# Kernel tuning notes

Hardware: AMD Instinct MI355X
Metric: run time of the kernel (lower is better)

## Reference

```python
import jax, jax.numpy as jnp
import numpy as np

SEQ_LEN, BATCH, INPUT, HID, LAYERS, TARGET_LEN = 120, 2048, 6, 64, 4, 120


def _cell(x_t, h, c, Wih, Whh, b):
    # torch LSTM gate order: input, forget, cell(g), output
    gates = x_t @ Wih.T + h @ Whh.T + b  # [B, 4H]
    i, f, g, o = jnp.split(gates, 4, axis=-1)
    c_new = jax.nn.sigmoid(f) * c + jax.nn.sigmoid(i) * jnp.tanh(g)
    h_new = jax.nn.sigmoid(o) * jnp.tanh(c_new)
    return h_new, c_new


def _stack_step(h, c, x_t, Wih0, Wih, Whh, b):
    # one time step through all stacked layers; h, c: [L, B, H]
    hs, cs = [], []
    inp = x_t
    L = Whh.shape[0]
    for l in range(L):
        W = Wih0 if l == 0 else Wih[l - 1]
        hn, cn = _cell(inp, h[l], c[l], W, Whh[l], b[l])
        hs.append(hn)
        cs.append(cn)
        inp = hn
    return jnp.stack(hs), jnp.stack(cs), inp


def setup_inputs() -> dict:
    key = jax.random.key(0)
    ks = jax.random.split(key, 11)
    s = 1.0 / np.sqrt(HID)  # torch LSTM uniform init scale
    u = lambda k, shp: jax.random.uniform(k, shp, jnp.float32, -s, s)
    return {
        "x": jax.random.normal(ks[0], (SEQ_LEN, BATCH, INPUT), jnp.float32),
        "enc_Wih0": u(ks[1], (4 * HID, INPUT)),
        "enc_Wih": u(ks[2], (LAYERS - 1, 4 * HID, HID)),
        "enc_Whh": u(ks[3], (LAYERS, 4 * HID, HID)),
        "enc_b": u(ks[4], (LAYERS, 4 * HID)),
        "dec_Wih0": u(ks[5], (4 * HID, INPUT)),
        "dec_Wih": u(ks[6], (LAYERS - 1, 4 * HID, HID)),
        "dec_Whh": u(ks[7], (LAYERS, 4 * HID, HID)),
        "dec_b": u(ks[8], (LAYERS, 4 * HID)),
        "lin_W": u(ks[9], (INPUT, HID)),
        "lin_b": u(ks[10], (INPUT,)),
        "target_len": TARGET_LEN,
    }


def reference(x, enc_Wih0, enc_Wih, enc_Whh, enc_b,
              dec_Wih0, dec_Wih, dec_Whh, dec_b, lin_W, lin_b, target_len):
    L, B, H = enc_Whh.shape[0], x.shape[1], enc_Whh.shape[-1]
    h0 = jnp.zeros((L, B, H), x.dtype)

    # ---- encoder: stacked LSTM over the input sequence (zero init state) ----
    def enc_step(carry, x_t):
        h, c = carry
        h, c, _ = _stack_step(h, c, x_t, enc_Wih0, enc_Wih, enc_Whh, enc_b)
        return (h, c), None

    (h, c), _ = jax.lax.scan(enc_step, (h0, h0), x)

    # ---- decoder: recursive one-step decode for target_len steps ----
    def dec_step(carry, _):
        h, c, inp = carry
        h, c, top = _stack_step(h, c, inp, dec_Wih0, dec_Wih, dec_Whh, dec_b)
        out = top @ lin_W.T + lin_b  # [B, INPUT]
        return (h, c, out), out

    last_in = x[-1]  # decoder seeded with last observed frame
    _, outputs = jax.lax.scan(dec_step, (h, c, last_in), None, length=target_len)
    return outputs  # [target_len, B, INPUT]
```

## Files before the change

kernel.cpp:

```cpp
#include <hip/hip_runtime.h>


#define S_LEN 120
#define BATCH 2048
#define NIN   6
#define H     64
#define NL    4
#define TLEN  120

#define HPAD 72
#define XPAD 40

#define FRAGS_HALF 60
#define PACK_H8    (2 * FRAGS_HALF * 4 * 64)
#define PROJ_H8    (2 * 64)
#define NPACK      ((PACK_H8 + PROJ_H8) * 8)

typedef _Float16 h8    __attribute__((ext_vector_type(8)));
typedef float    f32x4 __attribute__((ext_vector_type(4)));

__global__ void prep_weights(const float* __restrict__ eWih0,
                             const float* __restrict__ eWih,
                             const float* __restrict__ eWhh,
                             const float* __restrict__ dWih0,
                             const float* __restrict__ dWih,
                             const float* __restrict__ dWhh,
                             const float* __restrict__ linW,
                             _Float16* __restrict__ wq) {
  int idx = blockIdx.x * blockDim.x + threadIdx.x;
  if (idx >= NPACK) return;
  if (idx >= PACK_H8 * 8) {
    int p    = idx - PACK_H8 * 8;
    int j    = p & 7;
    int lane = (p >> 3) & 63;
    int kt   = p >> 9;
    int n    = lane & 15;
    int k    = kt * 32 + (lane >> 4) * 8 + j;
    wq[idx] = (_Float16)((n < NIN) ? linW[n * H + k] : 0.0f);
    return;
  }
  const int j    = idx & 7;
  const int lane = (idx >> 3) & 63;
  const int wv   = (idx >> 9) & 3;
  const int fh   = idx >> 11;
  const int f    = fh % FRAGS_HALF;
  const int half = fh / FRAGS_HALF;
  const float* Wi0 = half ? dWih0 : eWih0;
  const float* Wi  = half ? dWih  : eWih;
  const float* Wh  = half ? dWhh  : eWhh;

  int l, q, kt;
  if (f < 12) { l = 0; q = f / 3; kt = f % 3; }
  else        { int ff = f - 12; l = 1 + ff / 16; ff %= 16; q = ff / 4; kt = ff % 4; }

  const int g    = q * 64 + wv * 16 + (lane & 15);
  const int k_in = (lane >> 4) * 8 + j;
  float v;
  if (l == 0) {
    if (kt == 0) v = (k_in < NIN) ? Wi0[g * NIN + k_in] : 0.0f;
    else         v = Wh[g * H + (kt - 1) * 32 + k_in];
  } else {
    if (kt < 2) v = Wi[((l - 1) * 256 + g) * H + kt * 32 + k_in];
    else        v = Wh[(l * 256 + g) * H + (kt - 2) * 32 + k_in];
  }
  wq[idx] = (_Float16)v;
}

__device__ __forceinline__ float rcpf(float x) { return __builtin_amdgcn_rcpf(x); }
__device__ __forceinline__ float sigf(float x) { return rcpf(1.0f + __expf(-x)); }
__device__ __forceinline__ float tanhf_(float x) {
  float e = __expf(2.0f * x);
  return 1.0f - 2.0f * rcpf(e + 1.0f);
}
__device__ __forceinline__ f32x4 mf(h8 a, h8 b, f32x4 c) {
  return __builtin_amdgcn_mfma_f32_16x16x32_f16(a, b, c, 0, 0, 0);
}
#define SPLAT(v) ((f32x4){(v), (v), (v), (v)})

__device__ __forceinline__ void cell_ew(f32x4 g0, f32x4 g1, f32x4 g2, f32x4 g3,
                                        f32x4& c, _Float16* outbuf,
                                        int quad, int r16, int wv) {
  #pragma unroll
  for (int r = 0; r < 4; r++) {
    float gi = sigf(g0[r]);
    float gf = sigf(g1[r]);
    float gg = tanhf_(g2[r]);
    float go = sigf(g3[r]);
    c[r] = fmaf(gf, c[r], gi * gg);
    outbuf[(quad * 4 + r) * HPAD + wv * 16 + r16] = (_Float16)(go * tanhf_(c[r]));
  }
}

__device__ __forceinline__ void fireH(const h8 (&w)[16], h8 ai0, h8 ai1,
                                      const f32x4 (&ac)[4], f32x4& c,
                                      _Float16* outbuf, int quad, int r16, int wv) {
  f32x4 g0 = mf(ai1, w[1],  mf(ai0, w[0],  ac[0]));
  f32x4 g1 = mf(ai1, w[5],  mf(ai0, w[4],  ac[1]));
  f32x4 g2 = mf(ai1, w[9],  mf(ai0, w[8],  ac[2]));
  f32x4 g3 = mf(ai1, w[13], mf(ai0, w[12], ac[3]));
  cell_ew(g0, g1, g2, g3, c, outbuf, quad, r16, wv);
}
__device__ __forceinline__ void precH(const h8 (&w)[16], h8 ar0, h8 ar1,
                                      f32x4 b, f32x4 (&ac)[4]) {
  ac[0] = mf(ar1, w[3],  mf(ar0, w[2],  SPLAT(b[0])));
  ac[1] = mf(ar1, w[7],  mf(ar0, w[6],  SPLAT(b[1])));
  ac[2] = mf(ar1, w[11], mf(ar0, w[10], SPLAT(b[2])));
  ac[3] = mf(ar1, w[15], mf(ar0, w[14], SPLAT(b[3])));
}
__device__ __forceinline__ void fire0(const h8 (&w)[12], h8 ax,
                                      const f32x4 (&ac)[4], f32x4& c,
                                      _Float16* outbuf, int quad, int r16, int wv) {
  f32x4 g0 = mf(ax, w[0], ac[0]);
  f32x4 g1 = mf(ax, w[3], ac[1]);
  f32x4 g2 = mf(ax, w[6], ac[2]);
  f32x4 g3 = mf(ax, w[9], ac[3]);
  cell_ew(g0, g1, g2, g3, c, outbuf, quad, r16, wv);
}
__device__ __forceinline__ void prec0(const h8 (&w)[12], h8 ar0, h8 ar1,
                                      f32x4 b, f32x4 (&ac)[4]) {
  ac[0] = mf(ar1, w[2],  mf(ar0, w[1],  SPLAT(b[0])));
  ac[1] = mf(ar1, w[5],  mf(ar0, w[4],  SPLAT(b[1])));
  ac[2] = mf(ar1, w[8],  mf(ar0, w[7],  SPLAT(b[2])));
  ac[3] = mf(ar1, w[11], mf(ar0, w[10], SPLAT(b[3])));
}
__device__ __forceinline__ void readA(const _Float16* buf, int r16, int quad,
                                      h8& a0, h8& a1) {
  a0 = *(const h8*)(buf + r16 * HPAD + quad * 8);
  a1 = *(const h8*)(buf + r16 * HPAD + 32 + quad * 8);
}

__global__ void __launch_bounds__(256, 1)
lstm_main(const float* __restrict__ X,
          const float* __restrict__ encb,
          const float* __restrict__ decb,
          const float* __restrict__ linb,
          const h8* __restrict__ WQ,
          float* __restrict__ out) {
  __shared__ _Float16 Hb[NL][2][16][HPAD];
  __shared__ _Float16 Xb[2][16][XPAD];

  const int tid  = threadIdx.x;
  const int wv   = tid >> 6;
  const int lane = tid & 63;
  const int quad = lane >> 4;
  const int r16  = lane & 15;
  const int bbase = blockIdx.x * 16;

  {
    float* p = (float*)&Hb[0][0][0][0];
    for (int i = tid; i < (int)(NL * 2 * 16 * HPAD / 2); i += 256) p[i] = 0.0f;
    float* px = (float*)&Xb[0][0][0];
    for (int i = tid; i < (int)(2 * 16 * XPAD / 2); i += 256) px[i] = 0.0f;
  }
  if (tid < 96) {
    const int m = tid / NIN, i = tid - m * NIN;
    Xb[0][m][i] = (_Float16)X[((size_t)0 * BATCH + bbase + m) * NIN + i];
  }

  h8 w0[12], w1[16], w2[16], w3[16];
  #pragma unroll
  for (int f = 0; f < 12; f++) w0[f] = WQ[((f)      * 4 + wv) * 64 + lane];
  #pragma unroll
  for (int f = 0; f < 16; f++) w1[f] = WQ[((12 + f) * 4 + wv) * 64 + lane];
  #pragma unroll
  for (int f = 0; f < 16; f++) w2[f] = WQ[((28 + f) * 4 + wv) * 64 + lane];
  #pragma unroll
  for (int f = 0; f < 16; f++) w3[f] = WQ[((44 + f) * 4 + wv) * 64 + lane];

  f32x4 b0, b1, b2, b3;
  #pragma unroll
  for (int q = 0; q < 4; q++) {
    b0[q] = encb[0 * 256 + q * 64 + wv * 16 + r16];
    b1[q] = encb[1 * 256 + q * 64 + wv * 16 + r16];
    b2[q] = encb[2 * 256 + q * 64 + wv * 16 + r16];
    b3[q] = encb[3 * 256 + q * 64 + wv * 16 + r16];
  }

  f32x4 ac0[4], ac1[4], ac2[4], ac3[4];
  #pragma unroll
  for (int q = 0; q < 4; q++) {
    ac0[q] = SPLAT(b0[q]); ac1[q] = SPLAT(b1[q]);
    ac2[q] = SPLAT(b2[q]); ac3[q] = SPLAT(b3[q]);
  }

  f32x4 cs0 = SPLAT(0.f), cs1 = SPLAT(0.f), cs2 = SPLAT(0.f), cs3 = SPLAT(0.f);

  h8 lwf0 = {}, lwf1 = {};
  float lbv = 0.0f;
  if (wv == 0) {
    lwf0 = WQ[PACK_H8 + lane];
    lwf1 = WQ[PACK_H8 + 64 + lane];
    lbv  = (r16 < NIN) ? linb[r16] : 0.0f;
  }

  __syncthreads();

  #pragma unroll 1
  for (int t = 0; t < S_LEN; t++) {
    const int cur = t & 1, prv = cur ^ 1;
    {
      h8 ax = *(const h8*)(&Xb[cur][0][0] + r16 * XPAD + quad * 8);
      h8 ar0, ar1;
      readA(&Hb[3][prv][0][0], r16, quad, ar0, ar1);
      float xv = 0.0f; int pm = 0, pi = 0;
      const bool doPf = (tid < 96) && (t + 1 < S_LEN);
      if (doPf) {
        pm = tid / NIN; pi = tid - pm * NIN;
        xv = X[((size_t)(t + 1) * BATCH + bbase + pm) * NIN + pi];
      }
      fire0(w0, ax, ac0, cs0, &Hb[0][cur][0][0], quad, r16, wv);
      precH(w3, ar0, ar1, b3, ac3);
      __syncthreads();
      h8 ai0, ai1;
      readA(&Hb[0][cur][0][0], r16, quad, ai0, ai1);
      fireH(w1, ai0, ai1, ac1, cs1, &Hb[1][cur][0][0], quad, r16, wv);
      prec0(w0, ai0, ai1, b0, ac0);
      if (doPf) Xb[prv][pm][pi] = (_Float16)xv;
      __syncthreads();
      readA(&Hb[1][cur][0][0], r16, quad, ai0, ai1);
      fireH(w2, ai0, ai1, ac2, cs2, &Hb[2][cur][0][0], quad, r16, wv);
      precH(w1, ai0, ai1, b1, ac1);
      __syncthreads();
      readA(&Hb[2][cur][0][0], r16, quad, ai0, ai1);
      fireH(w3, ai0, ai1, ac3, cs3, &Hb[3][cur][0][0], quad, r16, wv);
      precH(w2, ai0, ai1, b2, ac2);
      __syncthreads();
    }
  }

  #pragma unroll
  for (int f = 0; f < 12; f++) w0[f] = WQ[((FRAGS_HALF + f)      * 4 + wv) * 64 + lane];
  #pragma unroll
  for (int f = 0; f < 16; f++) w1[f] = WQ[((FRAGS_HALF + 12 + f) * 4 + wv) * 64 + lane];
  #pragma unroll
  for (int f = 0; f < 16; f++) w2[f] = WQ[((FRAGS_HALF + 28 + f) * 4 + wv) * 64 + lane];
  #pragma unroll
  for (int f = 0; f < 16; f++) w3[f] = WQ[((FRAGS_HALF + 44 + f) * 4 + wv) * 64 + lane];
  #pragma unroll
  for (int q = 0; q < 4; q++) {
    b0[q] = decb[0 * 256 + q * 64 + wv * 16 + r16];
    b1[q] = decb[1 * 256 + q * 64 + wv * 16 + r16];
    b2[q] = decb[2 * 256 + q * 64 + wv * 16 + r16];
    b3[q] = decb[3 * 256 + q * 64 + wv * 16 + r16];
  }
  {
    h8 s0, s1;
    readA(&Hb[0][1][0][0], r16, quad, s0, s1); prec0(w0, s0, s1, b0, ac0);
    readA(&Hb[1][1][0][0], r16, quad, s0, s1); precH(w1, s0, s1, b1, ac1);
    readA(&Hb[2][1][0][0], r16, quad, s0, s1); precH(w2, s0, s1, b2, ac2);
    readA(&Hb[3][1][0][0], r16, quad, s0, s1); precH(w3, s0, s1, b3, ac3);
  }

  #pragma unroll 1
  for (int t = 0; t < TLEN; t++) {
    const int cur = t & 1, prv = cur ^ 1;
    {
      h8 ax = *(const h8*)(&Xb[prv][0][0] + r16 * XPAD + quad * 8);
      fire0(w0, ax, ac0, cs0, &Hb[0][cur][0][0], quad, r16, wv);
      __syncthreads();
      h8 ai0, ai1;
      readA(&Hb[0][cur][0][0], r16, quad, ai0, ai1);
      fireH(w1, ai0, ai1, ac1, cs1, &Hb[1][cur][0][0], quad, r16, wv);
      prec0(w0, ai0, ai1, b0, ac0);
      __syncthreads();
      readA(&Hb[1][cur][0][0], r16, quad, ai0, ai1);
      fireH(w2, ai0, ai1, ac2, cs2, &Hb[2][cur][0][0], quad, r16, wv);
      precH(w1, ai0, ai1, b1, ac1);
      __syncthreads();
      readA(&Hb[2][cur][0][0], r16, quad, ai0, ai1);
      fireH(w3, ai0, ai1, ac3, cs3, &Hb[3][cur][0][0], quad, r16, wv);
      precH(w2, ai0, ai1, b2, ac2);
      __syncthreads();
      h8 ar0, ar1;
      readA(&Hb[3][cur][0][0], r16, quad, ar0, ar1);
      precH(w3, ar0, ar1, b3, ac3);
      if (wv == 0) {
        f32x4 ap = SPLAT(lbv);
        ap = mf(ar0, lwf0, ap);
        ap = mf(ar1, lwf1, ap);
        if (r16 < NIN) {
          #pragma unroll
          for (int r = 0; r < 4; r++) {
            const int m = quad * 4 + r;
            out[((size_t)t * BATCH + bbase + m) * NIN + r16] = ap[r];
            Xb[cur][m][r16] = (_Float16)ap[r];
          }
        }
      }
      __syncthreads();
    }
  }
}

extern "C" void kernel_launch(void* const* d_in, const int* in_sizes, int n_in,
                              void* d_out, int out_size, void* d_ws, size_t ws_size,
                              hipStream_t stream) {
  const float* X     = (const float*)d_in[0];
  const float* eWih0 = (const float*)d_in[1];
  const float* eWih  = (const float*)d_in[2];
  const float* eWhh  = (const float*)d_in[3];
  const float* eb    = (const float*)d_in[4];
  const float* dWih0 = (const float*)d_in[5];
  const float* dWih  = (const float*)d_in[6];
  const float* dWhh  = (const float*)d_in[7];
  const float* db    = (const float*)d_in[8];
  const float* lW    = (const float*)d_in[9];
  const float* lb    = (const float*)d_in[10];

  _Float16* wq = (_Float16*)d_ws;

  prep_weights<<<(NPACK + 255) / 256, 256, 0, stream>>>(
      eWih0, eWih, eWhh, dWih0, dWih, dWhh, lW, wq);

  lstm_main<<<BATCH / 16, 256, 0, stream>>>(
      X, eb, db, lb, (const h8*)wq, (float*)d_out);
}
```

Measured before the change: 584.7 us.

## Wavefront-pipeline encoder layers across waves and drop the decoder's extra barrier

The encoder is restructured so each wave owns one LSTM layer and layers run as a diagonal wavefront over 123 steps, with one barrier per step instead of four. Each wave computes all 256 gates of its layer, using a new permuted weight packing and packed h4 stores. After the encoder, h and c are remapped into the decoder's layout through shared memory. In the decoder, every wave recomputes the output projection with transposed MFMA operands and passes the feedback input by lane shuffles, which removes the fifth barrier and the Xb round-trip. The cost is more weight registers per wave (64 h8 fragments), pipeline fill and drain steps, and remap overhead.

```diff
diff --git a/kernel.cpp b/kernel.cpp
--- a/kernel.cpp
+++ b/kernel.cpp
@@ -9,14 +9,19 @@
 #define TLEN  120
 
 #define HPAD 72
-#define XPAD 40
 
 #define FRAGS_HALF 60
 #define PACK_H8    (2 * FRAGS_HALF * 4 * 64)
 #define PROJ_H8    (2 * 64)
 #define NPACK      ((PACK_H8 + PROJ_H8) * 8)
+#define EPACK_EL   (256 * 64 * 8)
+#define NTOT       (NPACK + EPACK_EL)
+
+#define PERM(kk) ((((kk) & 3) << 4) | ((kk) >> 2))
+#define PI(c)    ((((c) & 15) << 2) | ((c) >> 4))
 
 typedef _Float16 h8    __attribute__((ext_vector_type(8)));
+typedef _Float16 h4    __attribute__((ext_vector_type(4)));
 typedef float    f32x4 __attribute__((ext_vector_type(4)));
 
 __global__ void prep_weights(const float* __restrict__ eWih0,
@@ -28,17 +33,42 @@
                              const float* __restrict__ linW,
                              _Float16* __restrict__ wq) {
   int idx = blockIdx.x * blockDim.x + threadIdx.x;
-  if (idx >= NPACK) return;
+  if (idx >= NTOT) return;
+
+  if (idx >= NPACK) {
+    int p    = idx - NPACK;
+    int j    = p & 7;
+    int lane = (p >> 3) & 63;
+    int fe   = p >> 9;
+    int kt   = fe & 3, nt = (fe >> 2) & 15, l = fe >> 6;
+    int g    = nt * 16 + (lane & 15);
+    int koff = ((lane >> 4) << 3) + j;
+    float v = 0.0f;
+    if (l == 0) {
+      if (kt == 0)      v = (koff < NIN) ? eWih0[g * NIN + koff] : 0.0f;
+      else if (kt == 1) v = 0.0f;
+      else { int kk = (kt - 2) * 32 + koff; v = eWhh[g * H + PERM(kk)]; }
+    } else {
+      if (kt < 2) { int kk = kt * 32 + koff;
+                    v = eWih[((l - 1) * 256 + g) * H + PERM(kk)]; }
+      else        { int kk = (kt - 2) * 32 + koff;
+                    v = eWhh[(l * 256 + g) * H + PERM(kk)]; }
+    }
+    wq[idx] = (_Float16)v;
+    return;
+  }
+
   if (idx >= PACK_H8 * 8) {
     int p    = idx - PACK_H8 * 8;
     int j    = p & 7;
     int lane = (p >> 3) & 63;
-    int kt   = p >> 9;
-    int n    = lane & 15;
-    int k    = kt * 32 + (lane >> 4) * 8 + j;
-    wq[idx] = (_Float16)((n < NIN) ? linW[n * H + k] : 0.0f);
+    int fr   = p >> 9;
+    int m    = lane & 15;
+    int k    = fr * 32 + ((lane >> 4) << 3) + j;
+    wq[idx] = (_Float16)((m < NIN) ? linW[m * H + k] : 0.0f);
     return;
   }
+
   const int j    = idx & 7;
   const int lane = (idx >> 3) & 63;
   const int wv   = (idx >> 9) & 3;
@@ -48,13 +78,11 @@
   const float* Wi0 = half ? dWih0 : eWih0;
   const float* Wi  = half ? dWih  : eWih;
   const float* Wh  = half ? dWhh  : eWhh;
-
   int l, q, kt;
   if (f < 12) { l = 0; q = f / 3; kt = f % 3; }
   else        { int ff = f - 12; l = 1 + ff / 16; ff %= 16; q = ff / 4; kt = ff % 4; }
-
   const int g    = q * 64 + wv * 16 + (lane & 15);
-  const int k_in = (lane >> 4) * 8 + j;
+  const int k_in = ((lane >> 4) << 3) + j;
   float v;
   if (l == 0) {
     if (kt == 0) v = (k_in < NIN) ? Wi0[g * NIN + k_in] : 0.0f;
@@ -90,7 +118,6 @@
     outbuf[(quad * 4 + r) * HPAD + wv * 16 + r16] = (_Float16)(go * tanhf_(c[r]));
   }
 }
-
 __device__ __forceinline__ void fireH(const h8 (&w)[16], h8 ai0, h8 ai1,
                                       const f32x4 (&ac)[4], f32x4& c,
                                       _Float16* outbuf, int quad, int r16, int wv) {
@@ -137,105 +164,142 @@
           const h8* __restrict__ WQ,
           float* __restrict__ out) {
   __shared__ _Float16 Hb[NL][2][16][HPAD];
-  __shared__ _Float16 Xb[2][16][XPAD];
-
-  const int tid  = threadIdx.x;
-  const int wv   = tid >> 6;
-  const int lane = tid & 63;
-  const int quad = lane >> 4;
-  const int r16  = lane & 15;
+  __shared__ _Float16 Xb[2][16][HPAD];
+  __shared__ float    Cx[NL][16][68];
+
+  const int tid   = threadIdx.x;
+  const int wv    = tid >> 6;
+  const int lane  = tid & 63;
+  const int quad  = lane >> 4;
+  const int r16   = lane & 15;
   const int bbase = blockIdx.x * 16;
 
   {
     float* p = (float*)&Hb[0][0][0][0];
     for (int i = tid; i < (int)(NL * 2 * 16 * HPAD / 2); i += 256) p[i] = 0.0f;
     float* px = (float*)&Xb[0][0][0];
-    for (int i = tid; i < (int)(2 * 16 * XPAD / 2); i += 256) px[i] = 0.0f;
+    for (int i = tid; i < (int)(2 * 16 * HPAD / 2); i += 256) px[i] = 0.0f;
   }
   if (tid < 96) {
     const int m = tid / NIN, i = tid - m * NIN;
     Xb[0][m][i] = (_Float16)X[((size_t)0 * BATCH + bbase + m) * NIN + i];
   }
 
+  h8 we[16][4];
+  #pragma unroll
+  for (int nt = 0; nt < 16; nt++)
+    #pragma unroll
+    for (int kt = 0; kt < 4; kt++)
+      we[nt][kt] = WQ[(PACK_H8 + PROJ_H8) + ((wv * 64 + nt * 4 + kt) * 64 + lane)];
+
+  float ben[16];
+  #pragma unroll
+  for (int nt = 0; nt < 16; nt++) ben[nt] = encb[wv * 256 + nt * 16 + r16];
+
+  f32x4 ce[4];
+  #pragma unroll
+  for (int ct = 0; ct < 4; ct++) ce[ct] = SPLAT(0.f);
+
+  __syncthreads();
+
+  #pragma unroll 1
+  for (int i = 0; i < S_LEN + NL - 1; i++) {
+    const int p = i & 1;
+    const bool active = (i >= wv) && (i - wv < S_LEN);
+    if (active) {
+      const _Float16* inb = (wv == 0) ? &Xb[p][0][0] : &Hb[wv - 1][p ^ 1][0][0];
+      const _Float16* rcb = &Hb[wv][p ^ 1][0][0];
+      h8 ai0 = *(const h8*)(inb + r16 * HPAD + quad * 8);
+      h8 ai1 = *(const h8*)(inb + r16 * HPAD + 32 + quad * 8);
+      h8 ar0 = *(const h8*)(rcb + r16 * HPAD + quad * 8);
+      h8 ar1 = *(const h8*)(rcb + r16 * HPAD + 32 + quad * 8);
+
+      float pf0 = 0.f, pf1 = 0.f;
+      const bool doPf = (wv == 0) && (lane < 48) && (i + 1 < S_LEN);
+      if (doPf) {
+        const float* xs = X + ((size_t)(i + 1) * BATCH + bbase) * NIN;
+        pf0 = xs[lane * 2];
+        pf1 = xs[lane * 2 + 1];
+      }
+
+      f32x4 acc[16];
+      #pragma unroll
+      for (int nt = 0; nt < 16; nt++) {
+        f32x4 a = SPLAT(ben[nt]);
+        a = mf(ai0, we[nt][0], a);
+        a = mf(ai1, we[nt][1], a);
+        a = mf(ar0, we[nt][2], a);
+        a = mf(ar1, we[nt][3], a);
+        acc[nt] = a;
+      }
+
+      _Float16* wb = &Hb[wv][p][0][0];
+      #pragma unroll
+      for (int r = 0; r < 4; r++) {
+        h4 hv;
+        #pragma unroll
+        for (int ct = 0; ct < 4; ct++) {
+          float gi = sigf(acc[ct][r]);
+          float gf = sigf(acc[4 + ct][r]);
+          float gg = tanhf_(acc[8 + ct][r]);
+          float go = sigf(acc[12 + ct][r]);
+          ce[ct][r] = fmaf(gf, ce[ct][r], gi * gg);
+          hv[ct] = (_Float16)(go * tanhf_(ce[ct][r]));
+        }
+        *(h4*)(wb + (quad * 4 + r) * HPAD + 4 * r16) = hv;
+      }
+
+      if (doPf) {
+        int e0 = lane * 2, e1 = e0 + 1;
+        Xb[p ^ 1][e0 / NIN][e0 % NIN] = (_Float16)pf0;
+        Xb[p ^ 1][e1 / NIN][e1 % NIN] = (_Float16)pf1;
+      }
+    }
+    __syncthreads();
+  }
+
+  #pragma unroll
+  for (int ct = 0; ct < 4; ct++)
+    #pragma unroll
+    for (int r = 0; r < 4; r++)
+      Cx[wv][quad * 4 + r][ct * 16 + r16] = ce[ct][r];
+
+  float hreg[16];
+  #pragma unroll
+  for (int u = 0; u < 16; u++) {
+    int i2 = tid + u * 256;
+    int l = i2 >> 10, m = (i2 >> 6) & 15, c = i2 & 63;
+    hreg[u] = (float)Hb[l][(l + 1) & 1][m][PI(c)];
+  }
+  __syncthreads();
+  #pragma unroll
+  for (int u = 0; u < 16; u++) {
+    int i2 = tid + u * 256;
+    int l = i2 >> 10, m = (i2 >> 6) & 15, c = i2 & 63;
+    Hb[l][1][m][c] = (_Float16)hreg[u];
+  }
+  __syncthreads();
+
+  f32x4 cs0, cs1, cs2, cs3;
+  #pragma unroll
+  for (int r = 0; r < 4; r++) {
+    cs0[r] = Cx[0][quad * 4 + r][wv * 16 + r16];
+    cs1[r] = Cx[1][quad * 4 + r][wv * 16 + r16];
+    cs2[r] = Cx[2][quad * 4 + r][wv * 16 + r16];
+    cs3[r] = Cx[3][quad * 4 + r][wv * 16 + r16];
+  }
+
   h8 w0[12], w1[16], w2[16], w3[16];
   #pragma unroll
-  for (int f = 0; f < 12; f++) w0[f] = WQ[((f)      * 4 + wv) * 64 + lane];
-  #pragma unroll
-  for (int f = 0; f < 16; f++) w1[f] = WQ[((12 + f) * 4 + wv) * 64 + lane];
-  #pragma unroll
-  for (int f = 0; f < 16; f++) w2[f] = WQ[((28 + f) * 4 + wv) * 64 + lane];
-  #pragma unroll
-  for (int f = 0; f < 16; f++) w3[f] = WQ[((44 + f) * 4 + wv) * 64 + lane];
+  for (int f = 0; f < 12; f++) w0[f] = WQ[((FRAGS_HALF + f)      * 4 + wv) * 64 + lane];
+  #pragma unroll
+  for (int f = 0; f < 16; f++) w1[f] = WQ[((FRAGS_HALF + 12 + f) * 4 + wv) * 64 + lane];
+  #pragma unroll
+  for (int f = 0; f < 16; f++) w2[f] = WQ[((FRAGS_HALF + 28 + f) * 4 + wv) * 64 + lane];
+  #pragma unroll
+  for (int f = 0; f < 16; f++) w3[f] = WQ[((FRAGS_HALF + 44 + f) * 4 + wv) * 64 + lane];
 
   f32x4 b0, b1, b2, b3;
-  #pragma unroll
-  for (int q = 0; q < 4; q++) {
-    b0[q] = encb[0 * 256 + q * 64 + wv * 16 + r16];
-    b1[q] = encb[1 * 256 + q * 64 + wv * 16 + r16];
-    b2[q] = encb[2 * 256 + q * 64 + wv * 16 + r16];
-    b3[q] = encb[3 * 256 + q * 64 + wv * 16 + r16];
-  }
-
-  f32x4 ac0[4], ac1[4], ac2[4], ac3[4];
-  #pragma unroll
-  for (int q = 0; q < 4; q++) {
-    ac0[q] = SPLAT(b0[q]); ac1[q] = SPLAT(b1[q]);
-    ac2[q] = SPLAT(b2[q]); ac3[q] = SPLAT(b3[q]);
-  }
-
-  f32x4 cs0 = SPLAT(0.f), cs1 = SPLAT(0.f), cs2 = SPLAT(0.f), cs3 = SPLAT(0.f);
-
-  h8 lwf0 = {}, lwf1 = {};
-  float lbv = 0.0f;
-  if (wv == 0) {
-    lwf0 = WQ[PACK_H8 + lane];
-    lwf1 = WQ[PACK_H8 + 64 + lane];
-    lbv  = (r16 < NIN) ? linb[r16] : 0.0f;
-  }
-
-  __syncthreads();
-
-  #pragma unroll 1
-  for (int t = 0; t < S_LEN; t++) {
-    const int cur = t & 1, prv = cur ^ 1;
-    {
-      h8 ax = *(const h8*)(&Xb[cur][0][0] + r16 * XPAD + quad * 8);
-      h8 ar0, ar1;
-      readA(&Hb[3][prv][0][0], r16, quad, ar0, ar1);
-      float xv = 0.0f; int pm = 0, pi = 0;
-      const bool doPf = (tid < 96) && (t + 1 < S_LEN);
-      if (doPf) {
-        pm = tid / NIN; pi = tid - pm * NIN;
-        xv = X[((size_t)(t + 1) * BATCH + bbase + pm) * NIN + pi];
-      }
-      fire0(w0, ax, ac0, cs0, &Hb[0][cur][0][0], quad, r16, wv);
-      precH(w3, ar0, ar1, b3, ac3);
-      __syncthreads();
-      h8 ai0, ai1;
-      readA(&Hb[0][cur][0][0], r16, quad, ai0, ai1);
-      fireH(w1, ai0, ai1, ac1, cs1, &Hb[1][cur][0][0], quad, r16, wv);
-      prec0(w0, ai0, ai1, b0, ac0);
-      if (doPf) Xb[prv][pm][pi] = (_Float16)xv;
-      __syncthreads();
-      readA(&Hb[1][cur][0][0], r16, quad, ai0, ai1);
-      fireH(w2, ai0, ai1, ac2, cs2, &Hb[2][cur][0][0], quad, r16, wv);
-      precH(w1, ai0, ai1, b1, ac1);
-      __syncthreads();
-      readA(&Hb[2][cur][0][0], r16, quad, ai0, ai1);
-      fireH(w3, ai0, ai1, ac3, cs3, &Hb[3][cur][0][0], quad, r16, wv);
-      precH(w2, ai0, ai1, b2, ac2);
-      __syncthreads();
-    }
-  }
-
-  #pragma unroll
-  for (int f = 0; f < 12; f++) w0[f] = WQ[((FRAGS_HALF + f)      * 4 + wv) * 64 + lane];
-  #pragma unroll
-  for (int f = 0; f < 16; f++) w1[f] = WQ[((FRAGS_HALF + 12 + f) * 4 + wv) * 64 + lane];
-  #pragma unroll
-  for (int f = 0; f < 16; f++) w2[f] = WQ[((FRAGS_HALF + 28 + f) * 4 + wv) * 64 + lane];
-  #pragma unroll
-  for (int f = 0; f < 16; f++) w3[f] = WQ[((FRAGS_HALF + 44 + f) * 4 + wv) * 64 + lane];
   #pragma unroll
   for (int q = 0; q < 4; q++) {
     b0[q] = decb[0 * 256 + q * 64 + wv * 16 + r16];
@@ -243,51 +307,94 @@
     b2[q] = decb[2 * 256 + q * 64 + wv * 16 + r16];
     b3[q] = decb[3 * 256 + q * 64 + wv * 16 + r16];
   }
+
+  h8 lwA0 = WQ[PACK_H8 + lane];
+  h8 lwA1 = WQ[PACK_H8 + 64 + lane];
+  f32x4 lbq;
+  #pragma unroll
+  for (int r = 0; r < 4; r++)
+    lbq[r] = (quad * 4 + r < NIN) ? linb[quad * 4 + r] : 0.0f;
+
+  f32x4 ac0[4], ac1[4], ac2[4], ac3[4];
   {
     h8 s0, s1;
     readA(&Hb[0][1][0][0], r16, quad, s0, s1); prec0(w0, s0, s1, b0, ac0);
     readA(&Hb[1][1][0][0], r16, quad, s0, s1); precH(w1, s0, s1, b1, ac1);
     readA(&Hb[2][1][0][0], r16, quad, s0, s1); precH(w2, s0, s1, b2, ac2);
-    readA(&Hb[3][1][0][0], r16, quad, s0, s1); precH(w3, s0, s1, b3, ac3);
-  }
+  }
+  __syncthreads();
 
   #pragma unroll 1
   for (int t = 0; t < TLEN; t++) {
     const int cur = t & 1, prv = cur ^ 1;
     {
-      h8 ax = *(const h8*)(&Xb[prv][0][0] + r16 * XPAD + quad * 8);
+      h8 ar0, ar1;
+      readA(&Hb[3][prv][0][0], r16, quad, ar0, ar1);
+      h8 ax;
+      if (t == 0) {
+        ax = *(const h8*)(&Xb[1][0][0] + r16 * HPAD + quad * 8);
+      } else {
+        f32x4 ap = lbq;
+        ap = mf(lwA0, ar0, ap);
+        ap = mf(lwA1, ar1, ap);
+        if (wv == 0) {
+          #pragma unroll
+          for (int r = 0; r < 4; r++) {
+            const int fm = quad * 4 + r;
+            if (fm < NIN)
+              out[((size_t)(t - 1) * BATCH + bbase + r16) * NIN + fm] = ap[r];
+          }
+        }
+        float x0 = __shfl(ap[0], r16);
+        float x1 = __shfl(ap[1], r16);
+        float x2 = __shfl(ap[2], r16);
+        float x3 = __shfl(ap[3], r16);
+        float x4 = __shfl(ap[0], 16 + r16);
+        float x5 = __shfl(ap[1], 16 + r16);
+        h8 xa = {};
+        xa[0] = (_Float16)x0; xa[1] = (_Float16)x1; xa[2] = (_Float16)x2;
+        xa[3] = (_Float16)x3; xa[4] = (_Float16)x4; xa[5] = (_Float16)x5;
+        h8 zz = {};
+        ax = (quad == 0) ? xa : zz;
+      }
+      precH(w3, ar0, ar1, b3, ac3);
       fire0(w0, ax, ac0, cs0, &Hb[0][cur][0][0], quad, r16, wv);
       __syncthreads();
+    }
+    {
       h8 ai0, ai1;
       readA(&Hb[0][cur][0][0], r16, quad, ai0, ai1);
       fireH(w1, ai0, ai1, ac1, cs1, &Hb[1][cur][0][0], quad, r16, wv);
       prec0(w0, ai0, ai1, b0, ac0);
       __syncthreads();
+    }
+    {
+      h8 ai0, ai1;
       readA(&Hb[1][cur][0][0], r16, quad, ai0, ai1);
       fireH(w2, ai0, ai1, ac2, cs2, &Hb[2][cur][0][0], quad, r16, wv);
       precH(w1, ai0, ai1, b1, ac1);
       __syncthreads();
+    }
+    {
+      h8 ai0, ai1;
       readA(&Hb[2][cur][0][0], r16, quad, ai0, ai1);
       fireH(w3, ai0, ai1, ac3, cs3, &Hb[3][cur][0][0], quad, r16, wv);
       precH(w2, ai0, ai1, b2, ac2);
       __syncthreads();
-      h8 ar0, ar1;
-      readA(&Hb[3][cur][0][0], r16, quad, ar0, ar1);
-      precH(w3, ar0, ar1, b3, ac3);
-      if (wv == 0) {
-        f32x4 ap = SPLAT(lbv);
-        ap = mf(ar0, lwf0, ap);
-        ap = mf(ar1, lwf1, ap);
-        if (r16 < NIN) {
-          #pragma unroll
-          for (int r = 0; r < 4; r++) {
-            const int m = quad * 4 + r;
-            out[((size_t)t * BATCH + bbase + m) * NIN + r16] = ap[r];
-            Xb[cur][m][r16] = (_Float16)ap[r];
-          }
-        }
-      }
-      __syncthreads();
+    }
+  }
+
+  if (wv == 0) {
+    h8 ar0, ar1;
+    readA(&Hb[3][1][0][0], r16, quad, ar0, ar1);
+    f32x4 ap = lbq;
+    ap = mf(lwA0, ar0, ap);
+    ap = mf(lwA1, ar1, ap);
+    #pragma unroll
+    for (int r = 0; r < 4; r++) {
+      const int fm = quad * 4 + r;
+      if (fm < NIN)
+        out[((size_t)(TLEN - 1) * BATCH + bbase + r16) * NIN + fm] = ap[r];
     }
   }
 }
@@ -309,7 +416,7 @@
 
   _Float16* wq = (_Float16*)d_ws;
 
-  prep_weights<<<(NPACK + 255) / 256, 256, 0, stream>>>(
+  prep_weights<<<(NTOT + 255) / 256, 256, 0, stream>>>(
       eWih0, eWih, eWhh, dWih0, dWih, dWhh, lW, wq);
 
   lstm_main<<<BATCH / 16, 256, 0, stream>>>(
```

Result: no change. 579.4 us (-0.9%).
